# Kernel tuning notes

Hardware: AMD Instinct MI355X
Metric: run time of the kernel (lower is better)

## Reference

```python
import jax, jax.numpy as jnp
import numpy as np

B, T, C = 4, 4096, 512
H, KS = 8, 9
D = C // H
PAD = KS // 2


def setup_inputs() -> dict:
    key = jax.random.key(0)
    ks = jax.random.split(key, 9)
    s = 1.0 / np.sqrt(C)
    return {
        "x": jax.random.normal(ks[0], (B, T, C), jnp.float32),
        "Wq": jax.random.normal(ks[1], (C, C), jnp.float32) * s,
        "bq": jax.random.normal(ks[2], (C,), jnp.float32) * 0.01,
        "Wk": jax.random.normal(ks[3], (C, C), jnp.float32) * s,
        "bk": jax.random.normal(ks[4], (C,), jnp.float32) * 0.01,
        "Wv": jax.random.normal(ks[5], (C, C), jnp.float32) * s,
        "bv": jax.random.normal(ks[6], (C,), jnp.float32) * 0.01,
        "Wo": jax.random.normal(ks[7], (C, C), jnp.float32) * s,
        "bo": jax.random.normal(ks[8], (C,), jnp.float32) * 0.01,
    }


def reference(x, Wq, bq, Wk, bk, Wv, bv, Wo, bo):
    Bx, Tx, Cx = x.shape
    # projections (torch Linear: x @ W.T + b), split heads -> (B,H,T,D)
    q = (x @ Wq.T + bq).reshape(Bx, Tx, H, D).transpose(0, 2, 1, 3)
    k = (x @ Wk.T + bk).reshape(Bx, Tx, H, D).transpose(0, 2, 1, 3)
    v = (x @ Wv.T + bv).reshape(Bx, Tx, H, D).transpose(0, 2, 1, 3)
    # replicate-pad along time (matches F.pad mode='replicate')
    k_pad = jnp.pad(k, ((0, 0), (0, 0), (PAD, PAD), (0, 0)), mode='edge')
    v_pad = jnp.pad(v, ((0, 0), (0, 0), (PAD, PAD), (0, 0)), mode='edge')
    # window gather indices: (T, KS) into padded time axis
    idx = jnp.arange(Tx)[:, None] + jnp.arange(KS)[None, :]
    k_unf = k_pad[:, :, idx, :]  # (B,H,T,KS,D)
    v_unf = v_pad[:, :, idx, :]  # (B,H,T,KS,D)
    scale = 1.0 / np.sqrt(D)
    scores = jnp.einsum('bhtd,bhtkd->bhtk', q, k_unf) * scale  # (B,H,T,KS)
    attn = jax.nn.softmax(scores, axis=-1)
    y = jnp.einsum('bhtk,bhtkd->bhtd', attn, v_unf)  # (B,H,T,D)
    y = y.transpose(0, 2, 1, 3).reshape(Bx, Tx, Cx)
    return y @ Wo.T + bo
```

## Files before the change

kernel.cpp:

```cpp
#include <hip/hip_runtime.h>
#include <hip/hip_bf16.h>

#define B_    4
#define T_    4096
#define C_    512
#define H_    8
#define D_    64
#define KS_   9
#define PAD_  4
#define MTOT  (B_ * T_)
#define PLANE (MTOT * C_)
#define WU    (C_ * C_ / 8)

typedef __bf16 bf16_t;
typedef __bf16 bf16x8 __attribute__((ext_vector_type(8)));
typedef float  f32x4  __attribute__((ext_vector_type(4)));

__global__ __launch_bounds__(256)
void conv_all(const float* __restrict__ Wq, const float* __restrict__ Wk,
              const float* __restrict__ Wv, const float* __restrict__ Wo,
              const float* __restrict__ x,
              bf16_t* __restrict__ Wb, bf16_t* __restrict__ xb) {
  int i = blockIdx.x * 256 + threadIdx.x;
  const float* src;
  bf16_t* dst;
  if (i < 4 * WU) {
    int w = i >> 15;
    const float* W = (w == 0) ? Wq : (w == 1) ? Wk : (w == 2) ? Wv : Wo;
    src = W + (size_t)(i & (WU - 1)) * 8;
    dst = Wb + (size_t)i * 8;
  } else {
    size_t j = (size_t)(i - 4 * WU);
    src = x + j * 8;
    dst = xb + j * 8;
  }
  float4 f0 = ((const float4*)src)[0];
  float4 f1 = ((const float4*)src)[1];
  bf16x8 o;
  o[0] = (bf16_t)f0.x; o[1] = (bf16_t)f0.y; o[2] = (bf16_t)f0.z; o[3] = (bf16_t)f0.w;
  o[4] = (bf16_t)f1.x; o[5] = (bf16_t)f1.y; o[6] = (bf16_t)f1.z; o[7] = (bf16_t)f1.w;
  *(bf16x8*)dst = o;
}

#define BM   256
#define BN   128
#define BK   64
#define NKT  (C_ / BK)
#define ASL  (BM * BK)

#define GLD(srcp, off) __builtin_amdgcn_global_load_lds(                     \
    (const __attribute__((address_space(1))) unsigned int*)(srcp),           \
    (__attribute__((address_space(3))) unsigned int*)(&sm[off]), 16, 0, 0)

template<int MODE>
__global__ __launch_bounds__(512, 2)
void gemm8p(const bf16_t* __restrict__ A, const bf16_t* __restrict__ Bw,
            const float* __restrict__ b0, const float* __restrict__ b1,
            const float* __restrict__ b2, void* __restrict__ Outp) {
  __shared__ __align__(16) bf16_t sm[3 * ASL];

  constexpr int GX  = (MODE == 0) ? (3 * C_ / BN) : (C_ / BN);
  constexpr int NWG = GX * (MTOT / BM);
  constexpr int CPX = NWG / 8;

  const int ord = blockIdx.y * GX + blockIdx.x;
  const int lg  = (ord & 7) * CPX + (ord >> 3);
  const int n0  = (lg % GX) * BN;
  const int m0  = (lg / GX) * BM;

  const int tid  = threadIdx.x;
  const int lane = tid & 63;
  const int wave = tid >> 6;
  const int wm   = wave >> 1;
  const int wn   = wave & 1;
  const int lr   = lane & 15;
  const int lq   = lane >> 4;

  const bf16_t* aSrc[4];
#pragma unroll
  for (int s = 0; s < 4; ++s) {
    int u = s * 512 + tid, r = u >> 3, ch = u & 7;
    int cs = (ch ^ (r & 7)) << 3;
    if constexpr (MODE == 0) {
      aSrc[s] = A + (size_t)(m0 + r) * C_ + cs;
    } else {
      int bb = m0 >> 12, t0 = m0 & (T_ - 1);
      aSrc[s] = A + ((size_t)bb * H_ * T_ + t0 + r) * D_ + cs;
    }
  }
  constexpr size_t ASTEP = (MODE == 0) ? (size_t)BK : (size_t)T_ * D_;

  const bf16_t* bBase[4];
#pragma unroll
  for (int j = 0; j < 4; ++j)
    bBase[j] = Bw + (size_t)(n0 + wn * 64 + j * 16 + lr) * C_ + lq * 8;

#pragma unroll
  for (int s = 0; s < 4; ++s) GLD(aSrc[s], (s * 512 + tid) * 8);
#pragma unroll
  for (int s = 0; s < 4; ++s) GLD(aSrc[s] + ASTEP, ASL + (s * 512 + tid) * 8);
  bf16x8 bfr[2][4][2];
#pragma unroll
  for (int j = 0; j < 4; ++j) {
    bfr[0][j][0] = *(const bf16x8*)(bBase[j]);
    bfr[0][j][1] = *(const bf16x8*)(bBase[j] + 32);
  }
  asm volatile("s_waitcnt vmcnt(12)" ::: "memory");
  __builtin_amdgcn_s_barrier();

  f32x4 acc[4][4] = {};
  const int co0 = ((0 + lq) ^ (lane & 7)) << 3;
  const int co1 = ((4 + lq) ^ (lane & 7)) << 3;

#pragma unroll
  for (int kt = 0; kt < NKT; ++kt) {
    const int rsl = kt % 3;
    const int wof = ((kt + 2) % 3) * ASL;
    const bf16_t* arow = &sm[rsl * ASL + (wm * 64 + lr) * 64];

    bf16x8 af[4][2];
#pragma unroll
    for (int i = 0; i < 4; ++i) {
      af[i][0] = *(const bf16x8*)(arow + i * 1024 + co0);
      af[i][1] = *(const bf16x8*)(arow + i * 1024 + co1);
    }
    if (kt + 2 < NKT) {
#pragma unroll
      for (int s = 0; s < 4; ++s)
        GLD(aSrc[s] + (size_t)(kt + 2) * ASTEP, wof + (s * 512 + tid) * 8);
    }
    if (kt + 1 < NKT) {
#pragma unroll
      for (int j = 0; j < 4; ++j) {
        bfr[(kt + 1) & 1][j][0] =
            *(const bf16x8*)(bBase[j] + (kt + 1) * 64);
        bfr[(kt + 1) & 1][j][1] =
            *(const bf16x8*)(bBase[j] + (kt + 1) * 64 + 32);
      }
    }
    __builtin_amdgcn_sched_barrier(0);
    asm volatile("s_waitcnt lgkmcnt(0)" ::: "memory");
    __builtin_amdgcn_sched_barrier(0);
    __builtin_amdgcn_s_setprio(1);
#pragma unroll
    for (int i = 0; i < 4; ++i)
#pragma unroll
      for (int j = 0; j < 4; ++j)
#pragma unroll
        for (int kk = 0; kk < 2; ++kk)
          acc[i][j] = __builtin_amdgcn_mfma_f32_16x16x32_bf16(
              af[i][kk], bfr[kt & 1][j][kk], acc[i][j], 0, 0, 0);
    __builtin_amdgcn_s_setprio(0);
    __builtin_amdgcn_sched_barrier(0);
    if (kt + 2 < NKT)      asm volatile("s_waitcnt vmcnt(12)" ::: "memory");
    else if (kt + 2 == NKT) asm volatile("s_waitcnt vmcnt(8)" ::: "memory");
    if (kt + 1 < NKT) __builtin_amdgcn_s_barrier();
  }

  const int cn = lane & 15;
  const int rq = (lane >> 4) << 2;
  if constexpr (MODE == 0) {
    const int z  = n0 >> 9;
    const float* bias = (z == 0) ? b0 : (z == 1) ? b1 : b2;
    const int bb = m0 >> 12;
    const int t0 = m0 & (T_ - 1);
    bf16_t* plane = (bf16_t*)Outp + (size_t)z * PLANE;
#pragma unroll
    for (int j = 0; j < 4; ++j) {
      const int cc  = (n0 & (C_ - 1)) + wn * 64 + j * 16 + cn;
      const int hh  = cc >> 6, dd = cc & 63;
      const float bvv = bias[cc];
      bf16_t* hb = plane + ((size_t)(bb * H_ + hh) * T_) * D_ + dd;
#pragma unroll
      for (int i = 0; i < 4; ++i)
#pragma unroll
        for (int r = 0; r < 4; ++r) {
          const int t = t0 + wm * 64 + i * 16 + rq + r;
          hb[(size_t)t * D_] = (bf16_t)(acc[i][j][r] + bvv);
        }
    }
  } else {
    float* outp = (float*)Outp;
#pragma unroll
    for (int j = 0; j < 4; ++j) {
      const int n = n0 + wn * 64 + j * 16 + cn;
      const float bvv = b0[n];
#pragma unroll
      for (int i = 0; i < 4; ++i)
#pragma unroll
        for (int r = 0; r < 4; ++r) {
          const int m = m0 + wm * 64 + i * 16 + rq + r;
          outp[(size_t)m * C_ + n] = acc[i][j][r] + bvv;
        }
    }
  }
}

__global__ __launch_bounds__(256)
void attn_kernel(const bf16_t* __restrict__ qkv, bf16_t* __restrict__ y) {
  const int tid  = threadIdx.x;
  const int sub  = tid & 7;
  const int tl   = tid >> 3;
  const int t    = blockIdx.x * 32 + tl;
  const int h    = blockIdx.y;
  const int b    = blockIdx.z;

  const size_t pl = (size_t)(b * H_ + h) * T_ * D_;
  const bf16_t* q = qkv + pl;
  const bf16_t* k = qkv + (size_t)PLANE + pl;
  const bf16_t* v = qkv + (size_t)2 * PLANE + pl;
  const int c = sub * 8;

  int tj[KS_];
#pragma unroll
  for (int j = 0; j < KS_; ++j) {
    int tt = t - PAD_ + j;
    tj[j] = tt < 0 ? 0 : (tt >= T_ ? T_ - 1 : tt);
  }

  bf16x8 q8 = *(const bf16x8*)(q + (size_t)t * D_ + c);
  float qf[8];
#pragma unroll
  for (int e = 0; e < 8; ++e) qf[e] = (float)q8[e];

  float s[KS_];
#pragma unroll
  for (int j = 0; j < KS_; ++j) {
    bf16x8 k8 = *(const bf16x8*)(k + (size_t)tj[j] * D_ + c);
    float d0 = 0.f;
#pragma unroll
    for (int e = 0; e < 8; ++e) d0 += qf[e] * (float)k8[e];
    s[j] = d0;
  }

#pragma unroll
  for (int m = 1; m < 8; m <<= 1)
#pragma unroll
    for (int j = 0; j < KS_; ++j) s[j] += __shfl_xor(s[j], m, 8);

  float mx = s[0];
#pragma unroll
  for (int j = 1; j < KS_; ++j) mx = fmaxf(mx, s[j]);
  float w[KS_], sum = 0.f;
#pragma unroll
  for (int j = 0; j < KS_; ++j) {
    w[j] = __expf((s[j] - mx) * 0.125f);
    sum += w[j];
  }
  const float inv = 1.f / sum;
#pragma unroll
  for (int j = 0; j < KS_; ++j) w[j] *= inv;

  float o[8] = {0.f, 0.f, 0.f, 0.f, 0.f, 0.f, 0.f, 0.f};
#pragma unroll
  for (int j = 0; j < KS_; ++j) {
    bf16x8 v8 = *(const bf16x8*)(v + (size_t)tj[j] * D_ + c);
#pragma unroll
    for (int e = 0; e < 8; ++e) o[e] += w[j] * (float)v8[e];
  }
  bf16x8 o8;
#pragma unroll
  for (int e = 0; e < 8; ++e) o8[e] = (bf16_t)o[e];
  *(bf16x8*)(y + pl + (size_t)t * D_ + c) = o8;
}

extern "C" void kernel_launch(void* const* d_in, const int* in_sizes, int n_in,
                              void* d_out, int out_size, void* d_ws, size_t ws_size,
                              hipStream_t stream) {
  const float* x  = (const float*)d_in[0];
  const float* Wq = (const float*)d_in[1];
  const float* bq = (const float*)d_in[2];
  const float* Wk = (const float*)d_in[3];
  const float* bk = (const float*)d_in[4];
  const float* Wv = (const float*)d_in[5];
  const float* bv = (const float*)d_in[6];
  const float* Wo = (const float*)d_in[7];
  const float* bo = (const float*)d_in[8];
  float* out = (float*)d_out;

  bf16_t* Wb  = (bf16_t*)d_ws;
  bf16_t* xb  = Wb + (size_t)4 * C_ * C_;
  bf16_t* qkv = xb + (size_t)PLANE;
  bf16_t* y   = xb;

  conv_all<<<(4 * WU + PLANE / 8) / 256, 256, 0, stream>>>(Wq, Wk, Wv, Wo, x, Wb, xb);
  gemm8p<0><<<dim3(3 * C_ / BN, MTOT / BM), 512, 0, stream>>>(
      xb, Wb, bq, bk, bv, qkv);
  attn_kernel<<<dim3(T_ / 32, H_, B_), 256, 0, stream>>>(qkv, y);
  gemm8p<1><<<dim3(C_ / BN, MTOT / BM), 512, 0, stream>>>(
      y, Wb + (size_t)3 * C_ * C_, bo, nullptr, nullptr, out);
}
```

Measured before the change: 207.4 us.

## Stage B tiles through LDS and shrink GEMM tiles to 128x128x32

```diff
diff --git a/kernel.cpp b/kernel.cpp
--- a/kernel.cpp
+++ b/kernel.cpp
@@ -42,22 +42,23 @@
   *(bf16x8*)dst = o;
 }
 
-#define BM   256
+#define BM   128
 #define BN   128
-#define BK   64
+#define BK   32
 #define NKT  (C_ / BK)
 #define ASL  (BM * BK)
+#define SLOT (2 * ASL)
 
 #define GLD(srcp, off) __builtin_amdgcn_global_load_lds(                     \
     (const __attribute__((address_space(1))) unsigned int*)(srcp),           \
     (__attribute__((address_space(3))) unsigned int*)(&sm[off]), 16, 0, 0)
 
 template<int MODE>
-__global__ __launch_bounds__(512, 2)
+__global__ __launch_bounds__(256, 3)
 void gemm8p(const bf16_t* __restrict__ A, const bf16_t* __restrict__ Bw,
             const float* __restrict__ b0, const float* __restrict__ b1,
             const float* __restrict__ b2, void* __restrict__ Outp) {
-  __shared__ __align__(16) bf16_t sm[3 * ASL];
+  __shared__ __align__(16) bf16_t sm[3 * SLOT];
 
   constexpr int GX  = (MODE == 0) ? (3 * C_ / BN) : (C_ / BN);
   constexpr int NWG = GX * (MTOT / BM);
@@ -76,67 +77,59 @@
   const int lr   = lane & 15;
   const int lq   = lane >> 4;
 
-  const bf16_t* aSrc[4];
-#pragma unroll
-  for (int s = 0; s < 4; ++s) {
-    int u = s * 512 + tid, r = u >> 3, ch = u & 7;
-    int cs = (ch ^ (r & 7)) << 3;
+  const bf16_t* aSrc[2];
+  const bf16_t* bSrc[2];
+#pragma unroll
+  for (int s = 0; s < 2; ++s) {
+    int u = s * 256 + tid, r = u >> 2, sl = u & 3;
+    int cs = (sl ^ ((r >> 1) & 3)) << 3;
     if constexpr (MODE == 0) {
       aSrc[s] = A + (size_t)(m0 + r) * C_ + cs;
     } else {
       int bb = m0 >> 12, t0 = m0 & (T_ - 1);
       aSrc[s] = A + ((size_t)bb * H_ * T_ + t0 + r) * D_ + cs;
     }
-  }
-  constexpr size_t ASTEP = (MODE == 0) ? (size_t)BK : (size_t)T_ * D_;
-
-  const bf16_t* bBase[4];
-#pragma unroll
-  for (int j = 0; j < 4; ++j)
-    bBase[j] = Bw + (size_t)(n0 + wn * 64 + j * 16 + lr) * C_ + lq * 8;
-
-#pragma unroll
-  for (int s = 0; s < 4; ++s) GLD(aSrc[s], (s * 512 + tid) * 8);
-#pragma unroll
-  for (int s = 0; s < 4; ++s) GLD(aSrc[s] + ASTEP, ASL + (s * 512 + tid) * 8);
-  bf16x8 bfr[2][4][2];
-#pragma unroll
-  for (int j = 0; j < 4; ++j) {
-    bfr[0][j][0] = *(const bf16x8*)(bBase[j]);
-    bfr[0][j][1] = *(const bf16x8*)(bBase[j] + 32);
-  }
-  asm volatile("s_waitcnt vmcnt(12)" ::: "memory");
+    bSrc[s] = Bw + (size_t)(n0 + r) * C_ + cs;
+  }
+  auto ofsA = [](int kt) -> size_t {
+    if constexpr (MODE == 0) return (size_t)kt * BK;
+    else return (size_t)(kt >> 1) * ((size_t)T_ * D_) + (size_t)(kt & 1) * 32;
+  };
+
+#pragma unroll
+  for (int s = 0; s < 2; ++s) GLD(aSrc[s] + ofsA(0), (s * 256 + tid) * 8);
+#pragma unroll
+  for (int s = 0; s < 2; ++s) GLD(bSrc[s], ASL + (s * 256 + tid) * 8);
+#pragma unroll
+  for (int s = 0; s < 2; ++s) GLD(aSrc[s] + ofsA(1), SLOT + (s * 256 + tid) * 8);
+#pragma unroll
+  for (int s = 0; s < 2; ++s) GLD(bSrc[s] + BK, SLOT + ASL + (s * 256 + tid) * 8);
+  asm volatile("s_waitcnt vmcnt(4)" ::: "memory");
   __builtin_amdgcn_s_barrier();
 
   f32x4 acc[4][4] = {};
-  const int co0 = ((0 + lq) ^ (lane & 7)) << 3;
-  const int co1 = ((4 + lq) ^ (lane & 7)) << 3;
+  const int co = ((lq ^ ((lr >> 1) & 3)) << 3);
 
 #pragma unroll
   for (int kt = 0; kt < NKT; ++kt) {
     const int rsl = kt % 3;
-    const int wof = ((kt + 2) % 3) * ASL;
-    const bf16_t* arow = &sm[rsl * ASL + (wm * 64 + lr) * 64];
-
-    bf16x8 af[4][2];
+    const int wof = ((kt + 2) % 3) * SLOT;
+    const bf16_t* abase = &sm[rsl * SLOT + (wm * 64 + lr) * BK + co];
+    const bf16_t* bbase = &sm[rsl * SLOT + ASL + (wn * 64 + lr) * BK + co];
+
+    bf16x8 af[4], bfr[4];
 #pragma unroll
     for (int i = 0; i < 4; ++i) {
-      af[i][0] = *(const bf16x8*)(arow + i * 1024 + co0);
-      af[i][1] = *(const bf16x8*)(arow + i * 1024 + co1);
+      af[i]  = *(const bf16x8*)(abase + i * (16 * BK));
+      bfr[i] = *(const bf16x8*)(bbase + i * (16 * BK));
     }
     if (kt + 2 < NKT) {
 #pragma unroll
-      for (int s = 0; s < 4; ++s)
-        GLD(aSrc[s] + (size_t)(kt + 2) * ASTEP, wof + (s * 512 + tid) * 8);
-    }
-    if (kt + 1 < NKT) {
-#pragma unroll
-      for (int j = 0; j < 4; ++j) {
-        bfr[(kt + 1) & 1][j][0] =
-            *(const bf16x8*)(bBase[j] + (kt + 1) * 64);
-        bfr[(kt + 1) & 1][j][1] =
-            *(const bf16x8*)(bBase[j] + (kt + 1) * 64 + 32);
-      }
+      for (int s = 0; s < 2; ++s)
+        GLD(aSrc[s] + ofsA(kt + 2), wof + (s * 256 + tid) * 8);
+#pragma unroll
+      for (int s = 0; s < 2; ++s)
+        GLD(bSrc[s] + (size_t)(kt + 2) * BK, wof + ASL + (s * 256 + tid) * 8);
     }
     __builtin_amdgcn_sched_barrier(0);
     asm volatile("s_waitcnt lgkmcnt(0)" ::: "memory");
@@ -146,14 +139,12 @@
     for (int i = 0; i < 4; ++i)
 #pragma unroll
       for (int j = 0; j < 4; ++j)
-#pragma unroll
-        for (int kk = 0; kk < 2; ++kk)
-          acc[i][j] = __builtin_amdgcn_mfma_f32_16x16x32_bf16(
-              af[i][kk], bfr[kt & 1][j][kk], acc[i][j], 0, 0, 0);
+        acc[i][j] = __builtin_amdgcn_mfma_f32_16x16x32_bf16(
+            af[i], bfr[j], acc[i][j], 0, 0, 0);
     __builtin_amdgcn_s_setprio(0);
     __builtin_amdgcn_sched_barrier(0);
-    if (kt + 2 < NKT)      asm volatile("s_waitcnt vmcnt(12)" ::: "memory");
-    else if (kt + 2 == NKT) asm volatile("s_waitcnt vmcnt(8)" ::: "memory");
+    if (kt + 2 < NKT)       asm volatile("s_waitcnt vmcnt(4)" ::: "memory");
+    else if (kt + 2 == NKT) asm volatile("s_waitcnt vmcnt(0)" ::: "memory");
     if (kt + 1 < NKT) __builtin_amdgcn_s_barrier();
   }
 
@@ -284,9 +275,9 @@
   bf16_t* y   = xb;
 
   conv_all<<<(4 * WU + PLANE / 8) / 256, 256, 0, stream>>>(Wq, Wk, Wv, Wo, x, Wb, xb);
-  gemm8p<0><<<dim3(3 * C_ / BN, MTOT / BM), 512, 0, stream>>>(
+  gemm8p<0><<<dim3(3 * C_ / BN, MTOT / BM), 256, 0, stream>>>(
       xb, Wb, bq, bk, bv, qkv);
   attn_kernel<<<dim3(T_ / 32, H_, B_), 256, 0, stream>>>(qkv, y);
-  gemm8p<1><<<dim3(C_ / BN, MTOT / BM), 512, 0, stream>>>(
+  gemm8p<1><<<dim3(C_ / BN, MTOT / BM), 256, 0, stream>>>(
       y, Wb + (size_t)3 * C_ * C_, bo, nullptr, nullptr, out);
 }
```

Measured after the change: 167.3 us. 1.24x faster.
